# Optimization experiments

Hardware: AMD Instinct MI355X
Metric: run time of the kernel (lower is better)

## Reference

```python
import jax, jax.numpy as jnp
import numpy as np

BATCH, SEQ, IN_DIM, OUT_DIM, N_STATE = 16, 4096, 64, 64, 512


def setup_inputs() -> dict:
    key = jax.random.key(0)
    k_x, k_a, k_b, k_c, k_d = jax.random.split(key, 5)
    x = jax.random.normal(k_x, (BATCH, SEQ, IN_DIM), dtype=jnp.float32)
    # Stable transition matrix: spectral-norm-ish scaling keeps h bounded over SEQ steps.
    A = jax.random.normal(k_a, (N_STATE, N_STATE), dtype=jnp.float32) * (0.9 / np.sqrt(N_STATE))
    B = jax.random.normal(k_b, (N_STATE, IN_DIM), dtype=jnp.float32) / np.sqrt(IN_DIM)
    C = jax.random.normal(k_c, (OUT_DIM, N_STATE), dtype=jnp.float32) / np.sqrt(N_STATE)
    D = jax.random.normal(k_d, (OUT_DIM, IN_DIM), dtype=jnp.float32) / np.sqrt(IN_DIM)
    return {"x": x, "A": A, "B": B, "C": C, "D": D}


def reference(x, A, B, C, D):
    """Linear SSM recurrence: h_t = A h_{t-1} + B x_t ; y_t = C h_t + D x_t.

    x: [batch, seq, in_dim] -> y: [batch, seq, out_dim]
    """
    batch = x.shape[0]
    n = A.shape[0]
    # Precompute input projections once (batched GEMMs outside the scan).
    bx = jnp.einsum("ni,bsi->sbn", B, x)   # [seq, batch, n_state]
    dx = jnp.einsum("oi,bsi->bso", D, x)   # [batch, seq, out_dim]

    def step(h, bx_t):
        # h: [batch, n_state]; bx_t: [batch, n_state]
        h_new = h @ A.T + bx_t
        return h_new, h_new

    h0 = jnp.zeros((batch, n), dtype=x.dtype)
    _, hs = jax.lax.scan(step, h0, bx)      # hs: [seq, batch, n_state]
    y = jnp.einsum("on,sbn->bso", C, hs) + dx
    return y
```

## Files before the change

### kernel.cpp

```cpp
#include <hip/hip_runtime.h>
#include <cstdint>
#include <cstddef>

#define BATCH 16
#define SEQ   4096
#define NS    512
#define TLAG  128
#define PADR  128
#define PS    (SEQ + PADR)
#define CTILE 128
#define XROWS (CTILE + TLAG - 1)
#define XSTR  72

typedef unsigned short u16;
typedef unsigned int   u32;
typedef short bf16x8 __attribute__((ext_vector_type(8)));
typedef float f32x4  __attribute__((ext_vector_type(4)));

__device__ __forceinline__ u16 f2bf(float f) {
    u32 u = __builtin_bit_cast(u32, f);
    return (u16)((u + 0x7FFFu + ((u >> 16) & 1u)) >> 16);
}
__device__ __forceinline__ float bf2f(u16 h) {
    return __builtin_bit_cast(float, (u32)h << 16);
}

__global__ __launch_bounds__(256) void prep_all(const float* __restrict__ x,
                                                const float* __restrict__ A,
                                                const float* __restrict__ B,
                                                const float* __restrict__ C,
                                                u16* __restrict__ xbf,
                                                u16* __restrict__ Ap0,
                                                u16* __restrict__ ApT0,
                                                u16* __restrict__ BT,
                                                u16* __restrict__ Wall)
{
    const int bid = blockIdx.x;
    if (bid < 4224) {
        const int id = bid * 256 + threadIdx.x;
        const int b   = id / (PS * 16);
        const int rem = id - b * (PS * 16);
        const int p   = rem >> 4;
        const int g   = id & 15;
        ushort4 o;
        if (p < PADR) {
            o.x = 0; o.y = 0; o.z = 0; o.w = 0;
        } else {
            const float4 v = *(const float4*)(x + ((size_t)b * SEQ + (p - PADR)) * 64 + g * 4);
            o.x = f2bf(v.x); o.y = f2bf(v.y); o.z = f2bf(v.z); o.w = f2bf(v.w);
        }
        *(ushort4*)(xbf + ((size_t)b * PS + p) * 64 + g * 4) = o;
    } else {
        const int id = (bid - 4224) * 256 + threadIdx.x;
        if (id < 262144) {
            const int r = id >> 9, c = id & 511;
            const u16 v = f2bf(A[id]);
            Ap0[id] = v;
            ApT0[(size_t)c * 512 + r] = v;
        } else if (id < 262144 + 32768) {
            const int i = id - 262144;
            const int k = i >> 6, c = i & 63;
            BT[(size_t)c * 512 + k] = f2bf(B[i]);
        } else if (id < 262144 + 65536) {
            const int i = id - 262144 - 32768;
            Wall[i] = f2bf(C[i]);
        }
    }
}

__device__ __forceinline__ void gemm_tile64(const u16* __restrict__ apM, int lda,
                                            const u16* __restrict__ bT, int ldbt, int n0,
                                            u16* __restrict__ oRM, int ldo,
                                            u16* __restrict__ oT, int ldoT, int rowT)
{
    const int tid = threadIdx.x;
    const int w = tid >> 6, l = tid & 63;
    const int lr = l & 15, q8 = (l >> 4) * 8;

    const u16* ap  = apM + (size_t)(w * 16 + lr) * lda + q8;
    const u16* bp0 = bT  + (size_t)(n0 + lr) * ldbt + q8;

    f32x4 acc[4];
    const f32x4 zero = {0.f, 0.f, 0.f, 0.f};
    #pragma unroll
    for (int nt = 0; nt < 4; ++nt) acc[nt] = zero;

    #pragma unroll 4
    for (int ks = 0; ks < 16; ++ks) {
        const bf16x8 a = *(const bf16x8*)(ap + ks * 32);
        #pragma unroll
        for (int nt = 0; nt < 4; ++nt) {
            const bf16x8 bfr = *(const bf16x8*)(bp0 + (size_t)nt * 16 * ldbt + ks * 32);
            acc[nt] = __builtin_amdgcn_mfma_f32_16x16x32_bf16(a, bfr, acc[nt], 0, 0, 0);
        }
    }

    const int rr = (l >> 4) * 4;
    #pragma unroll
    for (int nt = 0; nt < 4; ++nt) {
        const int col = n0 + nt * 16 + lr;
        if (oRM) {
            #pragma unroll
            for (int r = 0; r < 4; ++r)
                oRM[(size_t)(w * 16 + rr + r) * ldo + col] = f2bf(acc[nt][r]);
        }
        if (oT) {
            ushort4 pk;
            pk.x = f2bf(acc[nt][0]); pk.y = f2bf(acc[nt][1]);
            pk.z = f2bf(acc[nt][2]); pk.w = f2bf(acc[nt][3]);
            *(ushort4*)(oT + (size_t)col * ldoT + rowT + w * 16 + rr) = pk;
        }
    }
}

__global__ __launch_bounds__(256, 1) void level_kernel(u16* __restrict__ Wall,
                                                       const u16* __restrict__ Ap,
                                                       const u16* __restrict__ ApT,
                                                       u16* __restrict__ ApN,
                                                       u16* __restrict__ ApTN,
                                                       int h, int nexp)
{
    const int n0 = blockIdx.x * 64;
    const int by = blockIdx.y;
    if (by < nexp) {
        gemm_tile64(Wall + (size_t)by * 64 * NS, NS, ApT, NS, n0,
                    Wall + (size_t)(h + by) * 64 * NS, NS, nullptr, 0, 0);
    } else {
        const int j = by - nexp;
        gemm_tile64(Ap + (size_t)j * 64 * NS, NS, ApT, NS, n0,
                    ApN + (size_t)j * 64 * NS, NS, ApTN, NS, j * 64);
    }
}

__global__ __launch_bounds__(256, 1) void gfinal_kernel(const u16* __restrict__ Wall,
                                                        const u16* __restrict__ BT,
                                                        u16* __restrict__ Gtmp)
{
    gemm_tile64(Wall + (size_t)blockIdx.y * 64 * NS, NS, BT, NS, 0,
                Gtmp + (size_t)blockIdx.y * 64 * 64, 64, nullptr, 0, 0);
}

__global__ __launch_bounds__(256) void repack_g(const u16* __restrict__ Gtmp,
                                                const float* __restrict__ D,
                                                u16* __restrict__ Gsw)
{
    const int id = blockIdx.x * 256 + threadIdx.x;
    const int l  = id & 63;
    const int fi = id >> 6;
    const int m  = fi >> 3;
    const int ks = (fi >> 2) & 1;
    const int nt = fi & 3;
    const int o  = nt * 16 + (l & 15);
    const int q8 = (l >> 4) * 8;

    u16 v[8];
    #pragma unroll
    for (int j = 0; j < 8; ++j) {
        const int i = ks * 32 + q8 + j;
        u16 g = Gtmp[(size_t)(m * 64 + o) * 64 + i];
        if (m == 0) g = f2bf(bf2f(g) + D[o * 64 + i]);
        v[j] = g;
    }
    ushort4* dst = (ushort4*)(Gsw + (size_t)id * 8);
    ushort4 p0; p0.x = v[0]; p0.y = v[1]; p0.z = v[2]; p0.w = v[3];
    ushort4 p1; p1.x = v[4]; p1.y = v[5]; p1.z = v[6]; p1.w = v[7];
    dst[0] = p0; dst[1] = p1;
}

__global__ __launch_bounds__(256, 2) void conv_kernel(const u16* __restrict__ xbf,
                                                      const u16* __restrict__ gsw,
                                                      float* __restrict__ y)
{
    __shared__ u16 Xs[XROWS * XSTR];

    const int tid = threadIdx.x;
    const int b  = blockIdx.y;
    const int t0 = blockIdx.x * CTILE;

    {
        const int g = tid & 7;
        int r = tid >> 3;
        const u16* src = xbf + ((size_t)b * PS + t0 + 1) * 64 + g * 8;
        #pragma unroll
        for (int it = 0; it < 8; ++it, r += 32) {
            if (r < XROWS) {
                const uint4 v = *(const uint4*)(src + (size_t)r * 64);
                *(uint4*)&Xs[r * XSTR + g * 8] = v;
            }
        }
    }
    __syncthreads();

    const int w    = tid >> 6;
    const int l    = tid & 63;
    const int lr   = l & 15;
    const int q8   = (l >> 4) * 8;
    const int wrow = w * 32;

    const uint4* gp = (const uint4*)gsw + l;
    uint4 bn[8];
    #pragma unroll
    for (int f = 0; f < 8; ++f) bn[f] = gp[f * 64];

    f32x4 acc[2][4];
    const f32x4 zero = {0.f, 0.f, 0.f, 0.f};
    #pragma unroll
    for (int mt = 0; mt < 2; ++mt)
        #pragma unroll
        for (int nt = 0; nt < 4; ++nt) acc[mt][nt] = zero;

    #pragma unroll 2
    for (int m = 0; m < TLAG; ++m) {
        bf16x8 bc[8];
        #pragma unroll
        for (int f = 0; f < 8; ++f) bc[f] = __builtin_bit_cast(bf16x8, bn[f]);
        if (m < TLAG - 1) {
            const uint4* gn = gp + (size_t)(m + 1) * 512;
            #pragma unroll
            for (int f = 0; f < 8; ++f) bn[f] = gn[f * 64];
        }

        const int rbase = wrow + lr + (TLAG - 1) - m;
        bf16x8 a[2][2];
        #pragma unroll
        for (int mt = 0; mt < 2; ++mt)
            #pragma unroll
            for (int ks = 0; ks < 2; ++ks)
                a[mt][ks] = *(const bf16x8*)&Xs[(rbase + mt * 16) * XSTR + ks * 32 + q8];

        #pragma unroll
        for (int ks = 0; ks < 2; ++ks)
            #pragma unroll
            for (int mt = 0; mt < 2; ++mt)
                #pragma unroll
                for (int nt = 0; nt < 4; ++nt)
                    acc[mt][nt] = __builtin_amdgcn_mfma_f32_16x16x32_bf16(
                        a[mt][ks], bc[ks * 4 + nt], acc[mt][nt], 0, 0, 0);
    }

    const int rr = (l >> 4) * 4;
    #pragma unroll
    for (int mt = 0; mt < 2; ++mt) {
        #pragma unroll
        for (int nt = 0; nt < 4; ++nt) {
            const int t = t0 + wrow + mt * 16 + rr;
            const int o = nt * 16 + lr;
            float* yp = y + ((size_t)b * SEQ + t) * 64 + o;
            #pragma unroll
            for (int r = 0; r < 4; ++r) yp[(size_t)r * 64] = acc[mt][nt][r];
        }
    }
}

extern "C" void kernel_launch(void* const* d_in, const int* in_sizes, int n_in,
                              void* d_out, int out_size, void* d_ws, size_t ws_size,
                              hipStream_t stream)
{
    const float* x = (const float*)d_in[0];
    const float* A = (const float*)d_in[1];
    const float* B = (const float*)d_in[2];
    const float* C = (const float*)d_in[3];
    const float* D = (const float*)d_in[4];
    float* y = (float*)d_out;

    char* w = (char*)d_ws;
    u16* xbf    = (u16*)(w + 0);
    u16* Ap[2]  = { (u16*)(w + 8650752),  (u16*)(w + 9175040) };
    u16* ApT[2] = { (u16*)(w + 9699328),  (u16*)(w + 10223616) };
    u16* BT     = (u16*)(w + 10747904);
    u16* Wall   = (u16*)(w + 10813440);
    u16* Gtmp   = (u16*)(w + 19202048);
    u16* Gsw    = (u16*)(w + 20250624);

    prep_all<<<5504, 256, 0, stream>>>(x, A, B, C, xbf, Ap[0], ApT[0], BT, Wall);

    int h = 1, cur = 0;
    while (h < TLAG) {
        const int nexp = (h < TLAG - h) ? h : (TLAG - h);
        const int do_sq = (2 * h < TLAG) ? 1 : 0;
        dim3 grid(8, nexp + (do_sq ? 8 : 0));
        level_kernel<<<grid, 256, 0, stream>>>(Wall, Ap[cur], ApT[cur],
                                               Ap[cur ^ 1], ApT[cur ^ 1], h, nexp);
        if (do_sq) cur ^= 1;
        h += nexp;
    }

    gfinal_kernel<<<dim3(1, TLAG), 256, 0, stream>>>(Wall, BT, Gtmp);
    repack_g<<<256, 256, 0, stream>>>(Gtmp, D, Gsw);
    conv_kernel<<<dim3(SEQ / CTILE, BATCH), 256, 0, stream>>>(xbf, Gsw, y);
}
```

Before: 254.6 us.

## Fuse power-doubling GEMM levels into persistent kernel with global barriers

Replaces the sequence of per-level launches, the final G GEMM and the repack kernel with one persistent kernel. It runs two groups of 128 blocks, each group with its own copy of the W buffer, and the groups split the final expansion and G tiles between them. Levels are separated by atomic-counter global barriers, and stores use agent-scope atomic writes so other blocks see them. The goal is to remove kernel launch gaps and tail idle time across roughly ten small dependent launches. In exchange it relies on all 256 blocks being co-resident, and it adds barrier spin and duplicated work.

```diff
diff --git a/kernel.cpp b/kernel.cpp
--- a/kernel.cpp
+++ b/kernel.cpp
@@ -11,9 +11,11 @@
 #define CTILE 128
 #define XROWS (CTILE + TLAG - 1)
 #define XSTR  72
+#define GB    128
 
 typedef unsigned short u16;
 typedef unsigned int   u32;
+typedef unsigned long long u64;
 typedef short bf16x8 __attribute__((ext_vector_type(8)));
 typedef float f32x4  __attribute__((ext_vector_type(4)));
 
@@ -23,6 +25,11 @@
 }
 __device__ __forceinline__ float bf2f(u16 h) {
     return __builtin_bit_cast(float, (u32)h << 16);
+}
+
+__device__ __forceinline__ void wt_store(u16* p, ushort4 v) {
+    __hip_atomic_store((u64*)p, __builtin_bit_cast(u64, v),
+                       __ATOMIC_RELAXED, __HIP_MEMORY_SCOPE_AGENT);
 }
 
 __global__ __launch_bounds__(256) void prep_all(const float* __restrict__ x,
@@ -30,12 +37,15 @@
                                                 const float* __restrict__ B,
                                                 const float* __restrict__ C,
                                                 u16* __restrict__ xbf,
-                                                u16* __restrict__ Ap0,
-                                                u16* __restrict__ ApT0,
+                                                u16* __restrict__ Arm,
+                                                u16* __restrict__ At,
                                                 u16* __restrict__ BT,
-                                                u16* __restrict__ Wall)
+                                                u16* __restrict__ Wall0,
+                                                u16* __restrict__ Wall1,
+                                                u32* __restrict__ flg)
 {
     const int bid = blockIdx.x;
+    if (bid == 4224 && threadIdx.x < 64) flg[threadIdx.x] = 0;
     if (bid < 4224) {
         const int id = bid * 256 + threadIdx.x;
         const int b   = id / (PS * 16);
@@ -55,30 +65,46 @@
         if (id < 262144) {
             const int r = id >> 9, c = id & 511;
             const u16 v = f2bf(A[id]);
-            Ap0[id] = v;
-            ApT0[(size_t)c * 512 + r] = v;
+            Arm[id] = v;
+            At[(size_t)c * 512 + r] = v;
+            (void)r;
         } else if (id < 262144 + 32768) {
             const int i = id - 262144;
             const int k = i >> 6, c = i & 63;
             BT[(size_t)c * 512 + k] = f2bf(B[i]);
-        } else if (id < 262144 + 65536) {
-            const int i = id - 262144 - 32768;
-            Wall[i] = f2bf(C[i]);
-        }
-    }
-}
-
-__device__ __forceinline__ void gemm_tile64(const u16* __restrict__ apM, int lda,
-                                            const u16* __restrict__ bT, int ldbt, int n0,
-                                            u16* __restrict__ oRM, int ldo,
-                                            u16* __restrict__ oT, int ldoT, int rowT)
+        } else if (id < 262144 + 32768 + 131072) {
+            const int i  = id - 262144 - 32768;
+            const int gg = i >> 16;
+            const int ii = i & 65535;
+            const u16 v = f2bf(C[ii]);
+            if (gg == 0) Wall0[ii] = v; else Wall1[ii] = v;
+        }
+    }
+}
+
+__device__ __forceinline__ void gbar(u32* __restrict__ f)
+{
+    __syncthreads();
+    if (threadIdx.x == 0) {
+        __hip_atomic_fetch_add(f, 1u, __ATOMIC_RELAXED, __HIP_MEMORY_SCOPE_AGENT);
+        while (__hip_atomic_load(f, __ATOMIC_RELAXED, __HIP_MEMORY_SCOPE_AGENT) < (u32)GB)
+            __builtin_amdgcn_s_sleep(4);
+    }
+    __syncthreads();
+}
+
+__device__ __forceinline__ void gemm_wt(const u16* __restrict__ apM,
+                                        const u16* __restrict__ bT, int n0,
+                                        u16* __restrict__ oRM,
+                                        u16* __restrict__ oT, int rowT,
+                                        u16* __restrict__ lds)
 {
     const int tid = threadIdx.x;
     const int w = tid >> 6, l = tid & 63;
     const int lr = l & 15, q8 = (l >> 4) * 8;
 
-    const u16* ap  = apM + (size_t)(w * 16 + lr) * lda + q8;
-    const u16* bp0 = bT  + (size_t)(n0 + lr) * ldbt + q8;
+    const u16* ap  = apM + (size_t)(w * 16 + lr) * NS + q8;
+    const u16* bp0 = bT  + (size_t)(n0 + lr) * NS + q8;
 
     f32x4 acc[4];
     const f32x4 zero = {0.f, 0.f, 0.f, 0.f};
@@ -90,81 +116,154 @@
         const bf16x8 a = *(const bf16x8*)(ap + ks * 32);
         #pragma unroll
         for (int nt = 0; nt < 4; ++nt) {
-            const bf16x8 bfr = *(const bf16x8*)(bp0 + (size_t)nt * 16 * ldbt + ks * 32);
+            const bf16x8 bfr = *(const bf16x8*)(bp0 + (size_t)nt * 16 * NS + ks * 32);
             acc[nt] = __builtin_amdgcn_mfma_f32_16x16x32_bf16(a, bfr, acc[nt], 0, 0, 0);
         }
     }
 
     const int rr = (l >> 4) * 4;
-    #pragma unroll
-    for (int nt = 0; nt < 4; ++nt) {
-        const int col = n0 + nt * 16 + lr;
-        if (oRM) {
-            #pragma unroll
-            for (int r = 0; r < 4; ++r)
-                oRM[(size_t)(w * 16 + rr + r) * ldo + col] = f2bf(acc[nt][r]);
-        }
-        if (oT) {
+    if (oT) {
+        #pragma unroll
+        for (int nt = 0; nt < 4; ++nt) {
+            const int col = n0 + nt * 16 + lr;
             ushort4 pk;
             pk.x = f2bf(acc[nt][0]); pk.y = f2bf(acc[nt][1]);
             pk.z = f2bf(acc[nt][2]); pk.w = f2bf(acc[nt][3]);
-            *(ushort4*)(oT + (size_t)col * ldoT + rowT + w * 16 + rr) = pk;
-        }
-    }
-}
-
-__global__ __launch_bounds__(256, 1) void level_kernel(u16* __restrict__ Wall,
-                                                       const u16* __restrict__ Ap,
-                                                       const u16* __restrict__ ApT,
-                                                       u16* __restrict__ ApN,
-                                                       u16* __restrict__ ApTN,
-                                                       int h, int nexp)
-{
-    const int n0 = blockIdx.x * 64;
-    const int by = blockIdx.y;
-    if (by < nexp) {
-        gemm_tile64(Wall + (size_t)by * 64 * NS, NS, ApT, NS, n0,
-                    Wall + (size_t)(h + by) * 64 * NS, NS, nullptr, 0, 0);
-    } else {
-        const int j = by - nexp;
-        gemm_tile64(Ap + (size_t)j * 64 * NS, NS, ApT, NS, n0,
-                    ApN + (size_t)j * 64 * NS, NS, ApTN, NS, j * 64);
-    }
-}
-
-__global__ __launch_bounds__(256, 1) void gfinal_kernel(const u16* __restrict__ Wall,
-                                                        const u16* __restrict__ BT,
-                                                        u16* __restrict__ Gtmp)
-{
-    gemm_tile64(Wall + (size_t)blockIdx.y * 64 * NS, NS, BT, NS, 0,
-                Gtmp + (size_t)blockIdx.y * 64 * 64, 64, nullptr, 0, 0);
-}
-
-__global__ __launch_bounds__(256) void repack_g(const u16* __restrict__ Gtmp,
-                                                const float* __restrict__ D,
-                                                u16* __restrict__ Gsw)
-{
-    const int id = blockIdx.x * 256 + threadIdx.x;
-    const int l  = id & 63;
-    const int fi = id >> 6;
-    const int m  = fi >> 3;
-    const int ks = (fi >> 2) & 1;
-    const int nt = fi & 3;
-    const int o  = nt * 16 + (l & 15);
-    const int q8 = (l >> 4) * 8;
-
-    u16 v[8];
-    #pragma unroll
-    for (int j = 0; j < 8; ++j) {
-        const int i = ks * 32 + q8 + j;
-        u16 g = Gtmp[(size_t)(m * 64 + o) * 64 + i];
-        if (m == 0) g = f2bf(bf2f(g) + D[o * 64 + i]);
-        v[j] = g;
-    }
-    ushort4* dst = (ushort4*)(Gsw + (size_t)id * 8);
-    ushort4 p0; p0.x = v[0]; p0.y = v[1]; p0.z = v[2]; p0.w = v[3];
-    ushort4 p1; p1.x = v[4]; p1.y = v[5]; p1.z = v[6]; p1.w = v[7];
-    dst[0] = p0; dst[1] = p1;
+            wt_store(oT + (size_t)col * NS + rowT + w * 16 + rr, pk);
+        }
+    }
+    if (oRM) {
+        __syncthreads();
+        #pragma unroll
+        for (int nt = 0; nt < 4; ++nt)
+            #pragma unroll
+            for (int r = 0; r < 4; ++r)
+                lds[(w * 16 + rr + r) * 72 + nt * 16 + lr] = f2bf(acc[nt][r]);
+        __syncthreads();
+        const int r  = tid >> 2;
+        const int c0 = (tid & 3) * 16;
+        #pragma unroll
+        for (int k = 0; k < 4; ++k) {
+            const ushort4 q = *(const ushort4*)&lds[r * 72 + c0 + k * 4];
+            wt_store(oRM + (size_t)r * NS + n0 + c0 + k * 4, q);
+        }
+    }
+}
+
+__device__ __forceinline__ void g_tile(const u16* __restrict__ apW,
+                                       const u16* __restrict__ BT, int m,
+                                       const float* __restrict__ D,
+                                       u16* __restrict__ Gsw,
+                                       u16* __restrict__ lds)
+{
+    const int tid = threadIdx.x;
+    const int w = tid >> 6, l = tid & 63;
+    const int lr = l & 15, q8 = (l >> 4) * 8;
+
+    const u16* ap  = apW + (size_t)(w * 16 + lr) * NS + q8;
+    const u16* bp0 = BT  + (size_t)lr * NS + q8;
+
+    f32x4 acc[4];
+    const f32x4 zero = {0.f, 0.f, 0.f, 0.f};
+    #pragma unroll
+    for (int nt = 0; nt < 4; ++nt) acc[nt] = zero;
+
+    #pragma unroll 4
+    for (int ks = 0; ks < 16; ++ks) {
+        const bf16x8 a = *(const bf16x8*)(ap + ks * 32);
+        #pragma unroll
+        for (int nt = 0; nt < 4; ++nt) {
+            const bf16x8 bfr = *(const bf16x8*)(bp0 + (size_t)nt * 16 * NS + ks * 32);
+            acc[nt] = __builtin_amdgcn_mfma_f32_16x16x32_bf16(a, bfr, acc[nt], 0, 0, 0);
+        }
+    }
+
+    const int rr = (l >> 4) * 4;
+    __syncthreads();
+    #pragma unroll
+    for (int nt = 0; nt < 4; ++nt)
+        #pragma unroll
+        for (int r = 0; r < 4; ++r)
+            lds[(w * 16 + rr + r) * 72 + nt * 16 + lr] = f2bf(acc[nt][r]);
+    __syncthreads();
+
+    const int f = tid >> 6;
+    #pragma unroll
+    for (int f2 = 0; f2 < 8; f2 += 4) {
+        const int fi = f2 + f;
+        const int ks = fi >> 2, nt = fi & 3;
+        const int o  = nt * 16 + (l & 15);
+        const int i0 = ks * 32 + (l >> 4) * 8;
+        u16 v[8];
+        #pragma unroll
+        for (int j = 0; j < 8; ++j) {
+            u16 gv = lds[o * 72 + i0 + j];
+            if (m == 0) gv = f2bf(bf2f(gv) + D[o * 64 + i0 + j]);
+            v[j] = gv;
+        }
+        ushort4 p0; p0.x = v[0]; p0.y = v[1]; p0.z = v[2]; p0.w = v[3];
+        ushort4 p1; p1.x = v[4]; p1.y = v[5]; p1.z = v[6]; p1.w = v[7];
+        u16* dst = Gsw + ((size_t)(m * 8 + fi) * 64 + l) * 8;
+        wt_store(dst + 0, p0);
+        wt_store(dst + 4, p1);
+    }
+}
+
+__global__ __launch_bounds__(256, 1) void chain2(const float* __restrict__ D,
+                                                 const u16* __restrict__ Arm,
+                                                 const u16* __restrict__ At,
+                                                 const u16* __restrict__ BT,
+                                                 u16* __restrict__ S0,
+                                                 u16* __restrict__ Wall0,
+                                                 u16* __restrict__ Gsw,
+                                                 u32* __restrict__ flg)
+{
+    __shared__ u16 lds[64 * 72];
+
+    const int g    = blockIdx.x >> 7;
+    const int rank = blockIdx.x & (GB - 1);
+    u16* Sb = S0 + (size_t)g * 3145728;
+    u16* Wg = Wall0 + (size_t)g * 4194304;
+    u32* fg = flg + g * 16;
+
+    #pragma unroll 1
+    for (int lvl = 0; lvl < 6; ++lvl) {
+        const int h = 1 << lvl;
+        const u16* aSq = (lvl == 0) ? Arm : (Sb + (size_t)(lvl - 1) * 524288);
+        const u16* bTh = (lvl == 0) ? At  : (Sb + (size_t)(lvl - 1) * 524288 + 262144);
+        u16* SnRM = Sb + (size_t)lvl * 524288;
+        u16* SnT  = SnRM + 262144;
+        const int nexp8  = h * 8;
+        const int ntiles = nexp8 + 64;
+        for (int t = rank; t < ntiles; t += GB) {
+            if (t < nexp8) {
+                const int by = t >> 3, n0 = (t & 7) * 64;
+                gemm_wt(Wg + (size_t)by * 64 * NS, bTh, n0,
+                        Wg + (size_t)(h + by) * 64 * NS, nullptr, 0, lds);
+            } else {
+                const int tt = t - nexp8, mr = tt >> 3, n0 = (tt & 7) * 64;
+                gemm_wt(aSq + (size_t)mr * 64 * NS, bTh, n0,
+                        (lvl + 1 < 6) ? (SnRM + (size_t)mr * 64 * NS) : nullptr,
+                        SnT, mr * 64, lds);
+            }
+        }
+        gbar(&fg[lvl]);
+    }
+
+    {
+        const u16* S6t = Sb + (size_t)5 * 524288 + 262144;
+        for (int t = rank; t < 256; t += GB) {
+            const int by = 32 * g + (t >> 3), n0 = (t & 7) * 64;
+            gemm_wt(Wg + (size_t)by * 64 * NS, S6t, n0,
+                    Wg + (size_t)(64 + by) * 64 * NS, nullptr, 0, lds);
+        }
+        gbar(&fg[6]);
+    }
+
+    if (rank < 64) {
+        const int m = (rank < 32) ? (32 * g + rank) : (64 + 32 * g + rank - 32);
+        g_tile(Wg + (size_t)m * 64 * NS, BT, m, D, Gsw, lds);
+    }
 }
 
 __global__ __launch_bounds__(256, 2) void conv_kernel(const u16* __restrict__ xbf,
@@ -264,28 +363,17 @@
     float* y = (float*)d_out;
 
     char* w = (char*)d_ws;
-    u16* xbf    = (u16*)(w + 0);
-    u16* Ap[2]  = { (u16*)(w + 8650752),  (u16*)(w + 9175040) };
-    u16* ApT[2] = { (u16*)(w + 9699328),  (u16*)(w + 10223616) };
-    u16* BT     = (u16*)(w + 10747904);
-    u16* Wall   = (u16*)(w + 10813440);
-    u16* Gtmp   = (u16*)(w + 19202048);
-    u16* Gsw    = (u16*)(w + 20250624);
-
-    prep_all<<<5504, 256, 0, stream>>>(x, A, B, C, xbf, Ap[0], ApT[0], BT, Wall);
-
-    int h = 1, cur = 0;
-    while (h < TLAG) {
-        const int nexp = (h < TLAG - h) ? h : (TLAG - h);
-        const int do_sq = (2 * h < TLAG) ? 1 : 0;
-        dim3 grid(8, nexp + (do_sq ? 8 : 0));
-        level_kernel<<<grid, 256, 0, stream>>>(Wall, Ap[cur], ApT[cur],
-                                               Ap[cur ^ 1], ApT[cur ^ 1], h, nexp);
-        if (do_sq) cur ^= 1;
-        h += nexp;
-    }
-
-    gfinal_kernel<<<dim3(1, TLAG), 256, 0, stream>>>(Wall, BT, Gtmp);
-    repack_g<<<256, 256, 0, stream>>>(Gtmp, D, Gsw);
+    u16* xbf   = (u16*)(w + 0);
+    u16* Arm   = (u16*)(w + 8650752);
+    u16* At    = (u16*)(w + 9175040);
+    u16* BT    = (u16*)(w + 9699328);
+    u16* S0    = (u16*)(w + 9764864);
+    u16* Wall0 = (u16*)(w + 22347776);
+    u16* Wall1 = Wall0 + 4194304;
+    u16* Gsw   = (u16*)(w + 39124992);
+    u32* flg   = (u32*)(w + 40173568);
+
+    prep_all<<<5888, 256, 0, stream>>>(x, A, B, C, xbf, Arm, At, BT, Wall0, Wall1, flg);
+    chain2<<<256, 256, 0, stream>>>(D, Arm, At, BT, S0, Wall0, Gsw, flg);
     conv_kernel<<<dim3(SEQ / CTILE, BATCH), 256, 0, stream>>>(xbf, Gsw, y);
 }
```

After: 348.0 us. 1.37x slower.
